# Kernel tuning notes

Hardware: AMD Instinct MI355X
Metric: run time of the kernel (lower is better)

## Reference

```python
import jax, jax.numpy as jnp
import numpy as np

N_A, N_P, E = 50000, 50000, 600000
H, D = 8, 16
C = H * D  # hidden_channels = 128
OUT = 16
F_A, F_P = 256, 128
NEG_SLOPE = 0.2
EPS = 1e-5


def setup_inputs():
    key = jax.random.key(0)
    ks = jax.random.split(key, 16)
    return {
        'x_author': jax.random.normal(ks[0], (N_A, F_A), jnp.float32),
        'x_paper': jax.random.normal(ks[1], (N_P, F_P), jnp.float32),
        'W_a': jax.random.normal(ks[2], (F_A, C), jnp.float32) / np.sqrt(F_A).astype(np.float32),
        'b_a': jnp.zeros((C,), jnp.float32),
        'W_p': jax.random.normal(ks[3], (F_P, C), jnp.float32) / np.sqrt(F_P).astype(np.float32),
        'b_p': jnp.zeros((C,), jnp.float32),
        'att_src_ap': jax.random.normal(ks[4], (H, D), jnp.float32) * 0.1,
        'att_dst_ap': jax.random.normal(ks[5], (H, D), jnp.float32) * 0.1,
        'att_src_pp': jax.random.normal(ks[6], (H, D), jnp.float32) * 0.1,
        'att_dst_pp': jax.random.normal(ks[7], (H, D), jnp.float32) * 0.1,
        'k_W': jax.random.normal(ks[8], (C, C), jnp.float32) / np.sqrt(C).astype(np.float32),
        'k_b': jnp.zeros((C,), jnp.float32),
        'q': jax.random.normal(ks[9], (C,), jnp.float32) * 0.1,
        'norm_w': jnp.ones((C,), jnp.float32),
        'norm_b': jnp.zeros((C,), jnp.float32),
        'norm_ms': jnp.ones((C,), jnp.float32),
        'lin_W': jax.random.normal(ks[10], (C, OUT), jnp.float32) / np.sqrt(C).astype(np.float32),
        'lin_b': jnp.zeros((OUT,), jnp.float32),
        'edge_ap': jax.random.randint(ks[11], (2, E), 0, N_A),
        'edge_pp': jax.random.randint(ks[12], (2, E), 0, N_P),
    }


def _edge_type_out(h_src, h_dst, edge, a_src, a_dst, n_dst):
    # Node-level attention for one edge type (PyG HANConv per-metapath GAT).
    alpha_s = jnp.einsum('nhd,hd->nh', h_src, a_src)  # [N_src, H]
    alpha_d = jnp.einsum('nhd,hd->nh', h_dst, a_dst)  # [N_dst, H]
    src, dst = edge[0], edge[1]
    alpha = alpha_s[src] + alpha_d[dst]                       # [E, H]
    alpha = jnp.where(alpha >= 0, alpha, NEG_SLOPE * alpha)   # leaky_relu(0.2)
    m = jax.ops.segment_max(alpha, dst, num_segments=n_dst)
    e = jnp.exp(alpha - m[dst])
    denom = jax.ops.segment_sum(e, dst, num_segments=n_dst)
    attn = e / denom[dst]                                     # softmax over incoming edges
    msg = h_src[src] * attn[:, :, None]                       # [E, H, D]
    out = jax.ops.segment_sum(msg, dst, num_segments=n_dst)   # [n_dst, H, D]
    return jax.nn.relu(out.reshape(n_dst, H * D))


def reference(x_author, x_paper, W_a, b_a, W_p, b_p, att_src_ap, att_dst_ap,
              att_src_pp, att_dst_pp, k_W, k_b, q, norm_w, norm_b, norm_ms,
              lin_W, lin_b, edge_ap, edge_pp):
    # per-node-type projections -> [N, H, D]
    h_a = (x_author @ W_a + b_a).reshape(N_A, H, D)
    h_p = (x_paper @ W_p + b_p).reshape(N_P, H, D)
    # per-edge-type node-level attention + aggregation (both target 'paper')
    out_ap = _edge_type_out(h_a, h_p, edge_ap, att_src_ap, att_dst_ap, N_P)
    out_pp = _edge_type_out(h_p, h_p, edge_pp, att_src_pp, att_dst_pp, N_P)
    # semantic-level attention across the R=2 meta-paths
    outs = jnp.stack([out_ap, out_pp], axis=0)               # [R, N_P, C]
    w = jnp.tanh(outs @ k_W + k_b).mean(axis=1) @ q          # [R]
    beta = jax.nn.softmax(w)
    out = jnp.einsum('rnc,r->nc', outs, beta)                # [N_P, C]
    # GraphNorm (single graph: stats over all nodes)
    mean = out.mean(axis=0)
    o = out - mean * norm_ms
    var = (o * o).mean(axis=0)
    o = norm_w * o / jnp.sqrt(var + EPS) + norm_b
    # final classifier
    return o @ lin_W + lin_b
```

## Files before the change

### kernel.cpp

```cpp
#include <hip/hip_runtime.h>
#include <math.h>

#define NN   50000
#define EE   600000
#define CCH  128
#define HH   8
#define DD   16
#define OUTC 16
#define NEG  0.2f
#define EPSN 1e-5f
#define SLICE_DIV 12500
#define SCHUNKS 586
#define SCATB (SCHUNKS*8)
#define CAP 64
#define SBKT 32

typedef _Float16 f16x8 __attribute__((ext_vector_type(8)));
typedef float    f32x4 __attribute__((ext_vector_type(4)));

__device__ __forceinline__ float fast_tanh(float x) {
    x = fminf(10.f, fmaxf(-10.f, x));
    float e = __expf(2.f * x);
    return (e - 1.f) / (e + 1.f);
}

__global__ __launch_bounds__(256) void convw_k(const float* __restrict__ W_a,
        const float* __restrict__ W_p, const float* __restrict__ k_W,
        const float* __restrict__ lin_W, _Float16* __restrict__ Wt_a,
        _Float16* __restrict__ Wt_p, _Float16* __restrict__ kWt,
        _Float16* __restrict__ linWt)
{
    int id = blockIdx.x * 256 + threadIdx.x;
    if (id < 32768) {
        int k = id >> 7, n = id & 127;
        Wt_a[n * 256 + k] = (_Float16)W_a[id];
    } else if (id < 49152) {
        int i = id - 32768; int k = i >> 7, n = i & 127;
        Wt_p[n * 128 + k] = (_Float16)W_p[i];
    } else if (id < 65536) {
        int i = id - 49152; int k = i >> 7, n = i & 127;
        kWt[n * 128 + k] = (_Float16)k_W[i];
    } else if (id < 67584) {
        int i = id - 65536; int k = i >> 4, n = i & 15;
        linWt[n * 128 + k] = (_Float16)lin_W[i];
    }
}

__global__ __launch_bounds__(256) void gemm2h_k(const float* __restrict__ X_a,
        const float* __restrict__ X_p, const _Float16* __restrict__ Wt_a,
        const _Float16* __restrict__ Wt_p, const float* __restrict__ b_a,
        const float* __restrict__ b_p,
        const float* __restrict__ att_s_ap, const float* __restrict__ att_d_ap,
        const float* __restrict__ att_s_pp, const float* __restrict__ att_d_pp,
        _Float16* __restrict__ h_a, _Float16* __restrict__ h_p,
        float* __restrict__ as_ap, float* __restrict__ ad_ap,
        float* __restrict__ as_pp, float* __restrict__ ad_pp,
        const int* __restrict__ ea, const int* __restrict__ ep,
        int* __restrict__ fill, int* __restrict__ csrp, int GBn)
{
    __shared__ _Float16 As[64][40];
    __shared__ _Float16 Bs[128][40];
    const int t = threadIdx.x;
    const int G2 = 2 * GBn;
    const int TT = G2 + SCATB;
    const int b = (int)blockIdx.x;
    const int hi = (int)(((long long)(b + 1) * G2) / TT);
    const int lo = (int)(((long long)b * G2) / TT);
    if (hi == lo) {
        int bb = b - hi;
        int slice = bb & 7;
        int chunk = bb >> 3;
        int slo = slice * SLICE_DIV, shi = slo + SLICE_DIV;
        int base = chunk * 2048 + t;
        int d[8];
#pragma unroll
        for (int it = 0; it < 8; ++it) {
            int e = base + it * 256;
            int dd = -1;
            if (e < EE) dd = ea[EE + e];
            else if (e < 2 * EE) dd = NN + ep[e];
            d[it] = dd;
        }
#pragma unroll
        for (int it = 0; it < 8; ++it) {
            int dd = d[it];
            if (dd >= slo && dd < shi) {
                int e = base + it * 256;
                int pos = atomicAdd(&fill[dd], 1);
                if (pos < CAP) {
                    int s = (e < EE) ? ea[e] : ep[e - EE];
                    csrp[(size_t)dd * CAP + pos] = s;
                }
            }
        }
        return;
    }
    const int gb = lo;
    const int which = (gb >= GBn) ? 1 : 0;
    const float* X = which ? X_p : X_a;
    const _Float16* Wt = which ? Wt_p : Wt_a;
    const float* bias = which ? b_p : b_a;
    _Float16* Y = which ? h_p : h_a;
    const int K = which ? 128 : 256;
    const int r0 = (gb - which * GBn) * 64;
    const int lane = t & 63;
    const int wv = t >> 6;
    const int m16 = lane & 15;
    const int kq = lane >> 4;
    f32x4 acc[8];
#pragma unroll
    for (int i = 0; i < 8; ++i) acc[i] = (f32x4){0.f, 0.f, 0.f, 0.f};

    const int ar = t >> 2;
    const int ak = (t & 3) * 8;
    const int br = t >> 1;
    const int bk = (t & 1) * 16;

    for (int kc = 0; kc < K; kc += 32) {
        int row = r0 + ar;
        f16x8 av;
        if (row < NN) {
            const float4* gp = (const float4*)&X[row * K + kc + ak];
            float4 x0 = gp[0], x1 = gp[1];
            av[0] = (_Float16)x0.x; av[1] = (_Float16)x0.y;
            av[2] = (_Float16)x0.z; av[3] = (_Float16)x0.w;
            av[4] = (_Float16)x1.x; av[5] = (_Float16)x1.y;
            av[6] = (_Float16)x1.z; av[7] = (_Float16)x1.w;
        } else {
#pragma unroll
            for (int j = 0; j < 8; ++j) av[j] = (_Float16)0.f;
        }
        *(f16x8*)&As[ar][ak] = av;
        const f16x8* wp = (const f16x8*)&Wt[br * K + kc + bk];
        *(f16x8*)&Bs[br][bk]     = wp[0];
        *(f16x8*)&Bs[br][bk + 8] = wp[1];
        __syncthreads();
        f16x8 af = *(const f16x8*)&As[wv * 16 + m16][kq * 8];
#pragma unroll
        for (int i = 0; i < 8; ++i) {
            f16x8 bf = *(const f16x8*)&Bs[i * 16 + m16][kq * 8];
            acc[i] = __builtin_amdgcn_mfma_f32_16x16x32_f16(af, bf, acc[i], 0, 0, 0);
        }
        __syncthreads();
    }
    const int rbase = r0 + wv * 16 + kq * 4;
#pragma unroll
    for (int i = 0; i < 8; ++i) {
        int col = i * 16 + m16;
        float bv = bias[col];
        float hv[4];
#pragma unroll
        for (int rr = 0; rr < 4; ++rr) hv[rr] = acc[i][rr] + bv;
#pragma unroll
        for (int rr = 0; rr < 4; ++rr)
            if (rbase + rr < NN) Y[(rbase + rr) * 128 + col] = (_Float16)hv[rr];
        if (which == 0) {
            float av = att_s_ap[i * 16 + m16];
            float p[4];
#pragma unroll
            for (int rr = 0; rr < 4; ++rr) p[rr] = hv[rr] * av;
#pragma unroll
            for (int x = 1; x < 16; x <<= 1)
#pragma unroll
                for (int rr = 0; rr < 4; ++rr) p[rr] += __shfl_xor(p[rr], x, 64);
            if (m16 == 0) {
#pragma unroll
                for (int rr = 0; rr < 4; ++rr)
                    if (rbase + rr < NN) as_ap[(rbase + rr) * 8 + i] = p[rr];
            }
        } else {
            float a1 = att_d_ap[i * 16 + m16];
            float a2 = att_s_pp[i * 16 + m16];
            float a3 = att_d_pp[i * 16 + m16];
            float p1[4], p2[4], p3[4];
#pragma unroll
            for (int rr = 0; rr < 4; ++rr) {
                p1[rr] = hv[rr] * a1; p2[rr] = hv[rr] * a2; p3[rr] = hv[rr] * a3;
            }
#pragma unroll
            for (int x = 1; x < 16; x <<= 1) {
#pragma unroll
                for (int rr = 0; rr < 4; ++rr) {
                    p1[rr] += __shfl_xor(p1[rr], x, 64);
                    p2[rr] += __shfl_xor(p2[rr], x, 64);
                    p3[rr] += __shfl_xor(p3[rr], x, 64);
                }
            }
            if (m16 == 0) {
#pragma unroll
                for (int rr = 0; rr < 4; ++rr) {
                    if (rbase + rr < NN) {
                        ad_ap[(rbase + rr) * 8 + i] = p1[rr];
                        as_pp[(rbase + rr) * 8 + i] = p2[rr];
                        ad_pp[(rbase + rr) * 8 + i] = p3[rr];
                    }
                }
            }
        }
    }
}

__global__ __launch_bounds__(256) void agg4f_k(
        const _Float16* __restrict__ h_a, const _Float16* __restrict__ h_p,
        const float* __restrict__ as_ap, const float* __restrict__ ad_ap,
        const float* __restrict__ as_pp, const float* __restrict__ ad_pp,
        const int* __restrict__ fill, const int* __restrict__ csrp,
        const _Float16* __restrict__ kWt, const float* __restrict__ kb,
        const float* __restrict__ qv,
        _Float16* __restrict__ out_ap, _Float16* __restrict__ out_pp,
        float* __restrict__ wacc, float* __restrict__ statsb)
{
    __shared__ _Float16 Aap[16][136];
    __shared__ _Float16 App[16][136];
    __shared__ float sbuf[640];
    __shared__ float wred[4];
    const int t = threadIdx.x;
    const int wave = t >> 6, lane = t & 63;
    const int q = lane >> 4, sub = lane & 15;
    const int slot = wave * 4 + q;
    const int n = blockIdx.x * 16 + slot;
    const int h = sub >> 1;
    for (int i = t; i < 640; i += 256) sbuf[i] = 0.f;

    float oa[8], ob[8];
    {
        float adv = ad_ap[n * 8 + h];
        int cnt = fill[n]; if (cnt > CAP) cnt = CAP;
        const int* row = &csrp[(size_t)n * CAP];
        int p = 0;
        float l = 0.f;
        float acc[8] = {0.f,0.f,0.f,0.f,0.f,0.f,0.f,0.f};
        for (; p + 3 < cnt; p += 4) {
            int s0 = row[p], s1 = row[p+1], s2 = row[p+2], s3 = row[p+3];
            float a0 = as_ap[s0*8+h] + adv, a1 = as_ap[s1*8+h] + adv;
            float a2 = as_ap[s2*8+h] + adv, a3 = as_ap[s3*8+h] + adv;
            a0 = (a0 >= 0.f) ? a0 : NEG*a0; a1 = (a1 >= 0.f) ? a1 : NEG*a1;
            a2 = (a2 >= 0.f) ? a2 : NEG*a2; a3 = (a3 >= 0.f) ? a3 : NEG*a3;
            float w0 = __expf(a0), w1 = __expf(a1), w2 = __expf(a2), w3 = __expf(a3);
            f16x8 v0 = *(const f16x8*)&h_a[s0*CCH + sub*8];
            f16x8 v1 = *(const f16x8*)&h_a[s1*CCH + sub*8];
            f16x8 v2 = *(const f16x8*)&h_a[s2*CCH + sub*8];
            f16x8 v3 = *(const f16x8*)&h_a[s3*CCH + sub*8];
            l += (w0 + w1) + (w2 + w3);
#pragma unroll
            for (int i = 0; i < 8; ++i)
                acc[i] += (w0*(float)v0[i] + w1*(float)v1[i])
                        + (w2*(float)v2[i] + w3*(float)v3[i]);
        }
        for (; p < cnt; ++p) {
            int s0 = row[p];
            float a0 = as_ap[s0*8+h] + adv;
            a0 = (a0 >= 0.f) ? a0 : NEG*a0;
            float w0 = __expf(a0);
            f16x8 v0 = *(const f16x8*)&h_a[s0*CCH + sub*8];
            l += w0;
#pragma unroll
            for (int i = 0; i < 8; ++i) acc[i] += w0*(float)v0[i];
        }
        float inv = (l > 0.f) ? 1.f/l : 0.f;
#pragma unroll
        for (int i = 0; i < 8; ++i) oa[i] = fmaxf(acc[i]*inv, 0.f);
    }
    {
        float adv = ad_pp[n * 8 + h];
        int cnt = fill[NN + n]; if (cnt > CAP) cnt = CAP;
        const int* row = &csrp[(size_t)(NN + n) * CAP];
        int p = 0;
        float l = 0.f;
        float acc[8] = {0.f,0.f,0.f,0.f,0.f,0.f,0.f,0.f};
        for (; p + 3 < cnt; p += 4) {
            int s0 = row[p], s1 = row[p+1], s2 = row[p+2], s3 = row[p+3];
            float a0 = as_pp[s0*8+h] + adv, a1 = as_pp[s1*8+h] + adv;
            float a2 = as_pp[s2*8+h] + adv, a3 = as_pp[s3*8+h] + adv;
            a0 = (a0 >= 0.f) ? a0 : NEG*a0; a1 = (a1 >= 0.f) ? a1 : NEG*a1;
            a2 = (a2 >= 0.f) ? a2 : NEG*a2; a3 = (a3 >= 0.f) ? a3 : NEG*a3;
            float w0 = __expf(a0), w1 = __expf(a1), w2 = __expf(a2), w3 = __expf(a3);
            f16x8 v0 = *(const f16x8*)&h_p[s0*CCH + sub*8];
            f16x8 v1 = *(const f16x8*)&h_p[s1*CCH + sub*8];
            f16x8 v2 = *(const f16x8*)&h_p[s2*CCH + sub*8];
            f16x8 v3 = *(const f16x8*)&h_p[s3*CCH + sub*8];
            l += (w0 + w1) + (w2 + w3);
#pragma unroll
            for (int i = 0; i < 8; ++i)
                acc[i] += (w0*(float)v0[i] + w1*(float)v1[i])
                        + (w2*(float)v2[i] + w3*(float)v3[i]);
        }
        for (; p < cnt; ++p) {
            int s0 = row[p];
            float a0 = as_pp[s0*8+h] + adv;
            a0 = (a0 >= 0.f) ? a0 : NEG*a0;
            float w0 = __expf(a0);
            f16x8 v0 = *(const f16x8*)&h_p[s0*CCH + sub*8];
            l += w0;
#pragma unroll
            for (int i = 0; i < 8; ++i) acc[i] += w0*(float)v0[i];
        }
        float inv = (l > 0.f) ? 1.f/l : 0.f;
#pragma unroll
        for (int i = 0; i < 8; ++i) ob[i] = fmaxf(acc[i]*inv, 0.f);
    }
    f16x8 va, vb;
#pragma unroll
    for (int i = 0; i < 8; ++i) { va[i] = (_Float16)oa[i]; vb[i] = (_Float16)ob[i]; }
    *(f16x8*)&out_ap[n * CCH + sub * 8] = va;
    *(f16x8*)&out_pp[n * CCH + sub * 8] = vb;
    *(f16x8*)&Aap[slot][sub * 8] = va;
    *(f16x8*)&App[slot][sub * 8] = vb;
    float sa[8], sb[8], ssa[8], ssb[8], sab[8];
#pragma unroll
    for (int j = 0; j < 8; ++j) {
        float a = oa[j], bq = ob[j];
        sa[j] = a; sb[j] = bq; ssa[j] = a*a; ssb[j] = bq*bq; sab[j] = a*bq;
    }
#pragma unroll
    for (int x = 16; x < 64; x <<= 1) {
#pragma unroll
        for (int j = 0; j < 8; ++j) {
            sa[j]  += __shfl_xor(sa[j],  x, 64);
            sb[j]  += __shfl_xor(sb[j],  x, 64);
            ssa[j] += __shfl_xor(ssa[j], x, 64);
            ssb[j] += __shfl_xor(ssb[j], x, 64);
            sab[j] += __shfl_xor(sab[j], x, 64);
        }
    }
    __syncthreads();
    if (lane < 16) {
        int c0 = sub * 8;
#pragma unroll
        for (int j = 0; j < 8; ++j) {
            atomicAdd(&sbuf[c0 + j],       sa[j]);
            atomicAdd(&sbuf[128 + c0 + j], sb[j]);
            atomicAdd(&sbuf[256 + c0 + j], ssa[j]);
            atomicAdd(&sbuf[384 + c0 + j], ssb[j]);
            atomicAdd(&sbuf[512 + c0 + j], sab[j]);
        }
    }
    const int m16 = lane & 15, kq = lane >> 4;
    const int path = wave >> 1;
    float local = 0.f;
#pragma unroll
    for (int j = 0; j < 4; ++j) {
        int ct = (wave & 1) * 4 + j;
        f32x4 acc2 = (f32x4){0.f, 0.f, 0.f, 0.f};
#pragma unroll
        for (int kc = 0; kc < 128; kc += 32) {
            f16x8 af = path ? *(const f16x8*)&App[m16][kc + kq * 8]
                            : *(const f16x8*)&Aap[m16][kc + kq * 8];
            f16x8 bf = *(const f16x8*)&kWt[(ct * 16 + m16) * 128 + kc + kq * 8];
            acc2 = __builtin_amdgcn_mfma_f32_16x16x32_f16(af, bf, acc2, 0, 0, 0);
        }
        float kbc = kb[ct * 16 + m16], qc = qv[ct * 16 + m16];
#pragma unroll
        for (int rr = 0; rr < 4; ++rr)
            local += fast_tanh(acc2[rr] + kbc) * qc;
    }
#pragma unroll
    for (int x = 1; x < 64; x <<= 1) local += __shfl_xor(local, x, 64);
    if (lane == 0) wred[wave] = local;
    __syncthreads();
    if (t == 0) atomicAdd(&wacc[(blockIdx.x & 15) * 16],       wred[0] + wred[1]);
    if (t == 1) atomicAdd(&wacc[256 + (blockIdx.x & 15) * 16], wred[2] + wred[3]);
    if (t < 128) {
        float* sp = statsb + (size_t)(blockIdx.x & (SBKT - 1)) * 128;
        atomicAdd(&sp[t],                sbuf[t]);
        atomicAdd(&sp[SBKT*128 + t],     sbuf[128 + t]);
        atomicAdd(&sp[2*SBKT*128 + t],   sbuf[256 + t]);
        atomicAdd(&sp[3*SBKT*128 + t],   sbuf[384 + t]);
        atomicAdd(&sp[4*SBKT*128 + t],   sbuf[512 + t]);
    }
}

__global__ __launch_bounds__(256) void final2_k(
        const _Float16* __restrict__ oa, const _Float16* __restrict__ ob,
        const float* __restrict__ wacc, const float* __restrict__ statsb,
        const float* __restrict__ ms, const float* __restrict__ nw,
        const float* __restrict__ nb,
        const _Float16* __restrict__ linWt, const float* __restrict__ linb,
        float* __restrict__ out)
{
    __shared__ _Float16 As[64][136];
    __shared__ float scl[128], shf[128];
    __shared__ float bcoef[2];
    int t = threadIdx.x;
    if (t < 128) {
        float w0s = 0.f, w1s = 0.f;
#pragma unroll
        for (int i = 0; i < 16; ++i) {
            w0s += wacc[i * 16];
            w1s += wacc[256 + i * 16];
        }
        float w0 = w0s * (1.f / NN), w1 = w1s * (1.f / NN);
        float mm = fmaxf(w0, w1);
        float e0 = __expf(w0 - mm), e1 = __expf(w1 - mm);
        float b0 = e0 / (e0 + e1), b1 = e1 / (e0 + e1);
        if (t == 0) { bcoef[0] = b0; bcoef[1] = b1; }
        int c = t;
        float vsA = 0.f, vsB = 0.f, vssA = 0.f, vssB = 0.f, vsAB = 0.f;
        for (int i = 0; i < SBKT; ++i) {
            vsA  += statsb[i * 128 + c];
            vsB  += statsb[SBKT*128 + i * 128 + c];
            vssA += statsb[2*SBKT*128 + i * 128 + c];
            vssB += statsb[3*SBKT*128 + i * 128 + c];
            vsAB += statsb[4*SBKT*128 + i * 128 + c];
        }
        float mean = (b0 * vsA + b1 * vsB) * (1.f / NN);
        float ex2 = (b0 * b0 * vssA + 2.f * b0 * b1 * vsAB + b1 * b1 * vssB) * (1.f / NN);
        float a = mean * ms[c];
        float var = ex2 - 2.f * a * mean + a * a;
        float sc = nw[c] * rsqrtf(var + EPSN);
        scl[c] = sc;
        shf[c] = nb[c] - a * sc;
    }
    __syncthreads();
    float b0 = bcoef[0], b1 = bcoef[1];
    int r0 = blockIdx.x * 64;
    int row = t >> 2, cp = (t & 3) * 32;
    int gr = r0 + row;
    if (gr < NN) {
#pragma unroll
        for (int i = 0; i < 4; ++i) {
            int c0 = cp + i * 8;
            f16x8 va = *(const f16x8*)&oa[gr * CCH + c0];
            f16x8 vb = *(const f16x8*)&ob[gr * CCH + c0];
            f16x8 o;
#pragma unroll
            for (int e2 = 0; e2 < 8; ++e2) {
                float v = b0 * (float)va[e2] + b1 * (float)vb[e2];
                o[e2] = (_Float16)(v * scl[c0 + e2] + shf[c0 + e2]);
            }
            *(f16x8*)&As[row][c0] = o;
        }
    } else {
        f16x8 z;
#pragma unroll
        for (int e2 = 0; e2 < 8; ++e2) z[e2] = (_Float16)0.f;
#pragma unroll
        for (int i = 0; i < 4; ++i) *(f16x8*)&As[row][cp + i * 8] = z;
    }
    __syncthreads();
    int lane = t & 63, wv = t >> 6;
    int m16 = lane & 15, kq = lane >> 4;
    f32x4 acc = (f32x4){0.f, 0.f, 0.f, 0.f};
#pragma unroll
    for (int kc = 0; kc < 128; kc += 32) {
        f16x8 af = *(const f16x8*)&As[wv * 16 + m16][kc + kq * 8];
        f16x8 bf = *(const f16x8*)&linWt[m16 * 128 + kc + kq * 8];
        acc = __builtin_amdgcn_mfma_f32_16x16x32_f16(af, bf, acc, 0, 0, 0);
    }
    float lb = linb[m16];
#pragma unroll
    for (int r = 0; r < 4; ++r) {
        int gr2 = r0 + wv * 16 + kq * 4 + r;
        if (gr2 < NN) out[gr2 * 16 + m16] = acc[r] + lb;
    }
}

extern "C" void kernel_launch(void* const* d_in, const int* in_sizes, int n_in,
                              void* d_out, int out_size, void* d_ws, size_t ws_size,
                              hipStream_t stream) {
    const float* x_a   = (const float*)d_in[0];
    const float* x_p   = (const float*)d_in[1];
    const float* W_a   = (const float*)d_in[2];
    const float* b_a   = (const float*)d_in[3];
    const float* W_p   = (const float*)d_in[4];
    const float* b_p   = (const float*)d_in[5];
    const float* att_src_ap = (const float*)d_in[6];
    const float* att_dst_ap = (const float*)d_in[7];
    const float* att_src_pp = (const float*)d_in[8];
    const float* att_dst_pp = (const float*)d_in[9];
    const float* k_W   = (const float*)d_in[10];
    const float* k_b   = (const float*)d_in[11];
    const float* q     = (const float*)d_in[12];
    const float* norm_w = (const float*)d_in[13];
    const float* norm_b = (const float*)d_in[14];
    const float* norm_ms = (const float*)d_in[15];
    const float* lin_W = (const float*)d_in[16];
    const float* lin_b = (const float*)d_in[17];
    const int* edge_ap = (const int*)d_in[18];
    const int* edge_pp = (const int*)d_in[19];
    float* out = (float*)d_out;

    char* base = (char*)d_ws;
    size_t off = 0;
    auto alloc = [&](size_t bytes) -> void* {
        void* r = base + off;
        off += (bytes + 255) & ~(size_t)255;
        return r;
    };
    _Float16* h_a    = (_Float16*)alloc((size_t)NN * CCH * 2);
    _Float16* h_p    = (_Float16*)alloc((size_t)NN * CCH * 2);
    _Float16* out_ap = (_Float16*)alloc((size_t)NN * CCH * 2);
    _Float16* out_pp = (_Float16*)alloc((size_t)NN * CCH * 2);
    float* as_ap  = (float*)alloc((size_t)NN * HH * 4);
    float* ad_ap  = (float*)alloc((size_t)NN * HH * 4);
    float* as_pp  = (float*)alloc((size_t)NN * HH * 4);
    float* ad_pp  = (float*)alloc((size_t)NN * HH * 4);
    _Float16* Wt_a = (_Float16*)alloc((size_t)128 * 256 * 2);
    _Float16* Wt_p = (_Float16*)alloc((size_t)128 * 128 * 2);
    _Float16* kWt  = (_Float16*)alloc((size_t)128 * 128 * 2);
    _Float16* linWt = (_Float16*)alloc((size_t)16 * 128 * 2);
    int* csrp = (int*)alloc((size_t)2 * NN * CAP * 4);
    const size_t ZCOUNT = 100000 + 512 + 5 * SBKT * 128;
    int* zz = (int*)alloc(ZCOUNT * 4);
    int* fill   = zz;
    float* wacc = (float*)(zz + 100000);
    float* statsb = (float*)(zz + 100512);

    (void)in_sizes; (void)n_in; (void)out_size; (void)ws_size;

    hipMemsetAsync(zz, 0, ZCOUNT * 4, stream);

    convw_k<<<264, 256, 0, stream>>>(W_a, W_p, k_W, lin_W, Wt_a, Wt_p, kWt, linWt);

    const int GB = (NN + 63) / 64;
    gemm2h_k<<<2 * GB + SCATB, 256, 0, stream>>>(
        x_a, x_p, Wt_a, Wt_p, b_a, b_p,
        att_src_ap, att_dst_ap, att_src_pp, att_dst_pp,
        h_a, h_p, as_ap, ad_ap, as_pp, ad_pp,
        edge_ap, edge_pp, fill, csrp, GB);

    agg4f_k<<<NN / 16, 256, 0, stream>>>(h_a, h_p, as_ap, ad_ap, as_pp, ad_pp,
                                         fill, csrp, kWt, k_b, q,
                                         out_ap, out_pp, wacc, statsb);

    final2_k<<<GB, 256, 0, stream>>>(out_ap, out_pp, wacc, statsb,
                                     norm_ms, norm_w, norm_b, linWt, lin_b, out);
}
```

Measured before the change: 364.3 us.

## Drop sliced CSR scatter and interleave both edge-type aggregations

```diff
diff --git a/kernel.cpp b/kernel.cpp
--- a/kernel.cpp
+++ b/kernel.cpp
@@ -9,9 +9,7 @@
 #define OUTC 16
 #define NEG  0.2f
 #define EPSN 1e-5f
-#define SLICE_DIV 12500
 #define SCHUNKS 586
-#define SCATB (SCHUNKS*8)
 #define CAP 64
 #define SBKT 32
 
@@ -22,6 +20,10 @@
     x = fminf(10.f, fmaxf(-10.f, x));
     float e = __expf(2.f * x);
     return (e - 1.f) / (e + 1.f);
+}
+
+__device__ __forceinline__ float lrelu(float x) {
+    return (x >= 0.f) ? x : NEG * x;
 }
 
 __global__ __launch_bounds__(256) void convw_k(const float* __restrict__ W_a,
@@ -61,17 +63,9 @@
     __shared__ _Float16 As[64][40];
     __shared__ _Float16 Bs[128][40];
     const int t = threadIdx.x;
-    const int G2 = 2 * GBn;
-    const int TT = G2 + SCATB;
-    const int b = (int)blockIdx.x;
-    const int hi = (int)(((long long)(b + 1) * G2) / TT);
-    const int lo = (int)(((long long)b * G2) / TT);
-    if (hi == lo) {
-        int bb = b - hi;
-        int slice = bb & 7;
-        int chunk = bb >> 3;
-        int slo = slice * SLICE_DIV, shi = slo + SLICE_DIV;
-        int base = chunk * 2048 + t;
+    if ((int)blockIdx.x >= 2 * GBn) {
+        int bb = (int)blockIdx.x - 2 * GBn;
+        int base = bb * 2048 + t;
         int d[8];
 #pragma unroll
         for (int it = 0; it < 8; ++it) {
@@ -84,7 +78,7 @@
 #pragma unroll
         for (int it = 0; it < 8; ++it) {
             int dd = d[it];
-            if (dd >= slo && dd < shi) {
+            if (dd >= 0) {
                 int e = base + it * 256;
                 int pos = atomicAdd(&fill[dd], 1);
                 if (pos < CAP) {
@@ -95,14 +89,13 @@
         }
         return;
     }
-    const int gb = lo;
-    const int which = (gb >= GBn) ? 1 : 0;
+    const int which = ((int)blockIdx.x >= GBn) ? 1 : 0;
     const float* X = which ? X_p : X_a;
     const _Float16* Wt = which ? Wt_p : Wt_a;
     const float* bias = which ? b_p : b_a;
     _Float16* Y = which ? h_p : h_a;
     const int K = which ? 128 : 256;
-    const int r0 = (gb - which * GBn) * 64;
+    const int r0 = (blockIdx.x - which * GBn) * 64;
     const int lane = t & 63;
     const int wv = t >> 6;
     const int m16 = lane & 15;
@@ -222,82 +215,101 @@
     const int h = sub >> 1;
     for (int i = t; i < 640; i += 256) sbuf[i] = 0.f;
 
+    float adva = ad_ap[n * 8 + h];
+    float advp = ad_pp[n * 8 + h];
+    int cnt_a = fill[n];      if (cnt_a > CAP) cnt_a = CAP;
+    int cnt_p = fill[NN + n]; if (cnt_p > CAP) cnt_p = CAP;
+    const int* rowA = &csrp[(size_t)n * CAP];
+    const int* rowP = &csrp[(size_t)(NN + n) * CAP];
+    float la = 0.f, lp = 0.f;
+    float accA[8] = {0.f,0.f,0.f,0.f,0.f,0.f,0.f,0.f};
+    float accP[8] = {0.f,0.f,0.f,0.f,0.f,0.f,0.f,0.f};
+    int pa = 0, pb = 0;
+    while (pa + 3 < cnt_a && pb + 3 < cnt_p) {
+        int4 ra = *(const int4*)&rowA[pa];
+        int4 rp = *(const int4*)&rowP[pb];
+        float aa0 = as_ap[ra.x*8+h] + adva, aa1 = as_ap[ra.y*8+h] + adva;
+        float aa2 = as_ap[ra.z*8+h] + adva, aa3 = as_ap[ra.w*8+h] + adva;
+        float ap0 = as_pp[rp.x*8+h] + advp, ap1 = as_pp[rp.y*8+h] + advp;
+        float ap2 = as_pp[rp.z*8+h] + advp, ap3 = as_pp[rp.w*8+h] + advp;
+        float wa0 = __expf(lrelu(aa0)), wa1 = __expf(lrelu(aa1));
+        float wa2 = __expf(lrelu(aa2)), wa3 = __expf(lrelu(aa3));
+        float wp0 = __expf(lrelu(ap0)), wp1 = __expf(lrelu(ap1));
+        float wp2 = __expf(lrelu(ap2)), wp3 = __expf(lrelu(ap3));
+        f16x8 va0 = *(const f16x8*)&h_a[ra.x*CCH + sub*8];
+        f16x8 va1 = *(const f16x8*)&h_a[ra.y*CCH + sub*8];
+        f16x8 va2 = *(const f16x8*)&h_a[ra.z*CCH + sub*8];
+        f16x8 va3 = *(const f16x8*)&h_a[ra.w*CCH + sub*8];
+        f16x8 vp0 = *(const f16x8*)&h_p[rp.x*CCH + sub*8];
+        f16x8 vp1 = *(const f16x8*)&h_p[rp.y*CCH + sub*8];
+        f16x8 vp2 = *(const f16x8*)&h_p[rp.z*CCH + sub*8];
+        f16x8 vp3 = *(const f16x8*)&h_p[rp.w*CCH + sub*8];
+        la += (wa0 + wa1) + (wa2 + wa3);
+        lp += (wp0 + wp1) + (wp2 + wp3);
+#pragma unroll
+        for (int i = 0; i < 8; ++i) {
+            accA[i] += (wa0*(float)va0[i] + wa1*(float)va1[i])
+                     + (wa2*(float)va2[i] + wa3*(float)va3[i]);
+            accP[i] += (wp0*(float)vp0[i] + wp1*(float)vp1[i])
+                     + (wp2*(float)vp2[i] + wp3*(float)vp3[i]);
+        }
+        pa += 4; pb += 4;
+    }
+    for (; pa + 3 < cnt_a; pa += 4) {
+        int4 ra = *(const int4*)&rowA[pa];
+        float aa0 = as_ap[ra.x*8+h] + adva, aa1 = as_ap[ra.y*8+h] + adva;
+        float aa2 = as_ap[ra.z*8+h] + adva, aa3 = as_ap[ra.w*8+h] + adva;
+        float wa0 = __expf(lrelu(aa0)), wa1 = __expf(lrelu(aa1));
+        float wa2 = __expf(lrelu(aa2)), wa3 = __expf(lrelu(aa3));
+        f16x8 va0 = *(const f16x8*)&h_a[ra.x*CCH + sub*8];
+        f16x8 va1 = *(const f16x8*)&h_a[ra.y*CCH + sub*8];
+        f16x8 va2 = *(const f16x8*)&h_a[ra.z*CCH + sub*8];
+        f16x8 va3 = *(const f16x8*)&h_a[ra.w*CCH + sub*8];
+        la += (wa0 + wa1) + (wa2 + wa3);
+#pragma unroll
+        for (int i = 0; i < 8; ++i)
+            accA[i] += (wa0*(float)va0[i] + wa1*(float)va1[i])
+                     + (wa2*(float)va2[i] + wa3*(float)va3[i]);
+    }
+    for (; pa < cnt_a; ++pa) {
+        int s0 = rowA[pa];
+        float w0 = __expf(lrelu(as_ap[s0*8+h] + adva));
+        f16x8 v0 = *(const f16x8*)&h_a[s0*CCH + sub*8];
+        la += w0;
+#pragma unroll
+        for (int i = 0; i < 8; ++i) accA[i] += w0*(float)v0[i];
+    }
+    for (; pb + 3 < cnt_p; pb += 4) {
+        int4 rp = *(const int4*)&rowP[pb];
+        float ap0 = as_pp[rp.x*8+h] + advp, ap1 = as_pp[rp.y*8+h] + advp;
+        float ap2 = as_pp[rp.z*8+h] + advp, ap3 = as_pp[rp.w*8+h] + advp;
+        float wp0 = __expf(lrelu(ap0)), wp1 = __expf(lrelu(ap1));
+        float wp2 = __expf(lrelu(ap2)), wp3 = __expf(lrelu(ap3));
+        f16x8 vp0 = *(const f16x8*)&h_p[rp.x*CCH + sub*8];
+        f16x8 vp1 = *(const f16x8*)&h_p[rp.y*CCH + sub*8];
+        f16x8 vp2 = *(const f16x8*)&h_p[rp.z*CCH + sub*8];
+        f16x8 vp3 = *(const f16x8*)&h_p[rp.w*CCH + sub*8];
+        lp += (wp0 + wp1) + (wp2 + wp3);
+#pragma unroll
+        for (int i = 0; i < 8; ++i)
+            accP[i] += (wp0*(float)vp0[i] + wp1*(float)vp1[i])
+                     + (wp2*(float)vp2[i] + wp3*(float)vp3[i]);
+    }
+    for (; pb < cnt_p; ++pb) {
+        int s0 = rowP[pb];
+        float w0 = __expf(lrelu(as_pp[s0*8+h] + advp));
+        f16x8 v0 = *(const f16x8*)&h_p[s0*CCH + sub*8];
+        lp += w0;
+#pragma unroll
+        for (int i = 0; i < 8; ++i) accP[i] += w0*(float)v0[i];
+    }
+    float inva = (la > 0.f) ? 1.f/la : 0.f;
+    float invp = (lp > 0.f) ? 1.f/lp : 0.f;
     float oa[8], ob[8];
-    {
-        float adv = ad_ap[n * 8 + h];
-        int cnt = fill[n]; if (cnt > CAP) cnt = CAP;
-        const int* row = &csrp[(size_t)n * CAP];
-        int p = 0;
-        float l = 0.f;
-        float acc[8] = {0.f,0.f,0.f,0.f,0.f,0.f,0.f,0.f};
-        for (; p + 3 < cnt; p += 4) {
-            int s0 = row[p], s1 = row[p+1], s2 = row[p+2], s3 = row[p+3];
-            float a0 = as_ap[s0*8+h] + adv, a1 = as_ap[s1*8+h] + adv;
-            float a2 = as_ap[s2*8+h] + adv, a3 = as_ap[s3*8+h] + adv;
-            a0 = (a0 >= 0.f) ? a0 : NEG*a0; a1 = (a1 >= 0.f) ? a1 : NEG*a1;
-            a2 = (a2 >= 0.f) ? a2 : NEG*a2; a3 = (a3 >= 0.f) ? a3 : NEG*a3;
-            float w0 = __expf(a0), w1 = __expf(a1), w2 = __expf(a2), w3 = __expf(a3);
-            f16x8 v0 = *(const f16x8*)&h_a[s0*CCH + sub*8];
-            f16x8 v1 = *(const f16x8*)&h_a[s1*CCH + sub*8];
-            f16x8 v2 = *(const f16x8*)&h_a[s2*CCH + sub*8];
-            f16x8 v3 = *(const f16x8*)&h_a[s3*CCH + sub*8];
-            l += (w0 + w1) + (w2 + w3);
-#pragma unroll
-            for (int i = 0; i < 8; ++i)
-                acc[i] += (w0*(float)v0[i] + w1*(float)v1[i])
-                        + (w2*(float)v2[i] + w3*(float)v3[i]);
-        }
-        for (; p < cnt; ++p) {
-            int s0 = row[p];
-            float a0 = as_ap[s0*8+h] + adv;
-            a0 = (a0 >= 0.f) ? a0 : NEG*a0;
-            float w0 = __expf(a0);
-            f16x8 v0 = *(const f16x8*)&h_a[s0*CCH + sub*8];
-            l += w0;
-#pragma unroll
-            for (int i = 0; i < 8; ++i) acc[i] += w0*(float)v0[i];
-        }
-        float inv = (l > 0.f) ? 1.f/l : 0.f;
-#pragma unroll
-        for (int i = 0; i < 8; ++i) oa[i] = fmaxf(acc[i]*inv, 0.f);
-    }
-    {
-        float adv = ad_pp[n * 8 + h];
-        int cnt = fill[NN + n]; if (cnt > CAP) cnt = CAP;
-        const int* row = &csrp[(size_t)(NN + n) * CAP];
-        int p = 0;
-        float l = 0.f;
-        float acc[8] = {0.f,0.f,0.f,0.f,0.f,0.f,0.f,0.f};
-        for (; p + 3 < cnt; p += 4) {
-            int s0 = row[p], s1 = row[p+1], s2 = row[p+2], s3 = row[p+3];
-            float a0 = as_pp[s0*8+h] + adv, a1 = as_pp[s1*8+h] + adv;
-            float a2 = as_pp[s2*8+h] + adv, a3 = as_pp[s3*8+h] + adv;
-            a0 = (a0 >= 0.f) ? a0 : NEG*a0; a1 = (a1 >= 0.f) ? a1 : NEG*a1;
-            a2 = (a2 >= 0.f) ? a2 : NEG*a2; a3 = (a3 >= 0.f) ? a3 : NEG*a3;
-            float w0 = __expf(a0), w1 = __expf(a1), w2 = __expf(a2), w3 = __expf(a3);
-            f16x8 v0 = *(const f16x8*)&h_p[s0*CCH + sub*8];
-            f16x8 v1 = *(const f16x8*)&h_p[s1*CCH + sub*8];
-            f16x8 v2 = *(const f16x8*)&h_p[s2*CCH + sub*8];
-            f16x8 v3 = *(const f16x8*)&h_p[s3*CCH + sub*8];
-            l += (w0 + w1) + (w2 + w3);
-#pragma unroll
-            for (int i = 0; i < 8; ++i)
-                acc[i] += (w0*(float)v0[i] + w1*(float)v1[i])
-                        + (w2*(float)v2[i] + w3*(float)v3[i]);
-        }
-        for (; p < cnt; ++p) {
-            int s0 = row[p];
-            float a0 = as_pp[s0*8+h] + adv;
-            a0 = (a0 >= 0.f) ? a0 : NEG*a0;
-            float w0 = __expf(a0);
-            f16x8 v0 = *(const f16x8*)&h_p[s0*CCH + sub*8];
-            l += w0;
-#pragma unroll
-            for (int i = 0; i < 8; ++i) acc[i] += w0*(float)v0[i];
-        }
-        float inv = (l > 0.f) ? 1.f/l : 0.f;
-#pragma unroll
-        for (int i = 0; i < 8; ++i) ob[i] = fmaxf(acc[i]*inv, 0.f);
+#pragma unroll
+    for (int i = 0; i < 8; ++i) {
+        oa[i] = fmaxf(accA[i]*inva, 0.f);
+        ob[i] = fmaxf(accP[i]*invp, 0.f);
     }
     f16x8 va, vb;
 #pragma unroll
@@ -513,7 +525,7 @@
     convw_k<<<264, 256, 0, stream>>>(W_a, W_p, k_W, lin_W, Wt_a, Wt_p, kWt, linWt);
 
     const int GB = (NN + 63) / 64;
-    gemm2h_k<<<2 * GB + SCATB, 256, 0, stream>>>(
+    gemm2h_k<<<2 * GB + SCHUNKS, 256, 0, stream>>>(
         x_a, x_p, Wt_a, Wt_p, b_a, b_p,
         att_src_ap, att_dst_ap, att_src_pp, att_dst_pp,
         h_a, h_p, as_ap, ad_ap, as_pp, ad_pp,
```

Result: slower. 372.9 us (+2.4%).
